# Kernel optimization log

Hardware: AMD Instinct MI355X
Metric: run time of the kernel (lower is better)

## Reference

```python
import jax, jax.numpy as jnp
import numpy as np

NUM_GENES = 978
EMBED_DIM = 301
NUM_HEADS = 4
EMBED_DIM_HEADS = 48
N_NODES = 10000
N_EDGES = 320000


def setup_inputs() -> dict:
    key = jax.random.key(0)
    k1, k2, k3, k4 = jax.random.split(key, 4)
    x = jax.random.normal(k1, (N_NODES, NUM_GENES), dtype=jnp.float32)
    edge_index = jax.random.randint(k2, (2, N_EDGES), 0, N_NODES, dtype=jnp.int64)
    edge_weight = jax.random.uniform(k3, (N_EDGES,), dtype=jnp.float32)
    # GCNConv params: glorot-ish linear weight and zero bias
    W = jax.random.normal(k4, (NUM_GENES, EMBED_DIM), dtype=jnp.float32) * 0.03
    b = jnp.zeros((EMBED_DIM,), dtype=jnp.float32)
    return {"x": x, "edge_index": edge_index, "edge_weight": edge_weight, "W": W, "b": b}


def reference(x, edge_index, edge_weight, W, b):
    N = x.shape[0]
    src, dst = edge_index[0], edge_index[1]
    # GCNConv default: add self-loops with weight 1
    loop = jnp.arange(N, dtype=src.dtype)
    src_f = jnp.concatenate([src, loop])
    dst_f = jnp.concatenate([dst, loop])
    w_f = jnp.concatenate([edge_weight, jnp.ones((N,), dtype=edge_weight.dtype)])
    # symmetric normalization: deg over target nodes
    deg = jax.ops.segment_sum(w_f, dst_f, num_segments=N)
    deg_inv_sqrt = jnp.where(deg > 0, jax.lax.rsqrt(deg), 0.0)
    norm = deg_inv_sqrt[src_f] * w_f * deg_inv_sqrt[dst_f]  # [E+N]
    h = x @ W  # [N, EMBED_DIM]
    # gather source features, scale, scatter-add into targets
    out = jax.ops.segment_sum(norm[:, None] * h[src_f], dst_f, num_segments=N)
    out = out + b
    out = jax.nn.relu(out)
    # unsqueeze(1), unsqueeze(3), repeat(1, H, 1, dph) with H=4, dph=48//4=12
    rep = EMBED_DIM_HEADS // NUM_HEADS
    out = jnp.broadcast_to(out[:, None, :, None], (N, NUM_HEADS, EMBED_DIM, rep))
    return out
```

## Files before the change

### kernel.cpp

```cpp
#include <hip/hip_runtime.h>
#include <math.h>

#define NGENES 978
#define EDIM   301
#define NNODES 10000
#define NEDGES 320000
#define KPAD   992
#define NPAD   320
#define MPAD   10112
#define HP     320
#define ELLS   128

typedef float f4v __attribute__((ext_vector_type(4)));
typedef short s8v __attribute__((ext_vector_type(8)));

__device__ __forceinline__ void split_bf16(float v, short& hi, short& lo) {
    unsigned int b = __float_as_uint(v);
    hi = (short)(b >> 16);
    float hif = __uint_as_float(b & 0xFFFF0000u);
    float lof = v - hif;
    lo = (short)(__float_as_uint(lof) >> 16);
}

__global__ void prep_init(const unsigned int* __restrict__ ei, int* flag, int* cur) {
    int i = blockIdx.x * blockDim.x + threadIdx.x;
    if (i < NNODES) cur[i] = 0;
    if (blockIdx.x == 0 && threadIdx.x < 64) {
        unsigned int v = ei[2 * threadIdx.x + 1];
        unsigned long long nz = __ballot(v != 0u);
        if (threadIdx.x == 0) *flag = (nz == 0ULL) ? 1 : 0;
    }
}

__device__ __forceinline__ int load_idx(const void* ei, long long i, int is64) {
    return is64 ? (int)((const long long*)ei)[i] : ((const int*)ei)[i];
}

__global__ void fill_ell(const void* __restrict__ ei, const float* __restrict__ w,
                         int* cur, int2* __restrict__ ell,
                         const int* __restrict__ flag) {
    int e = blockIdx.x * blockDim.x + threadIdx.x;
    if (e >= NEDGES) return;
    int is64 = *flag;
    int s = load_idx(ei, e, is64);
    int d = load_idx(ei, (long long)NEDGES + e, is64);
    int slot = atomicAdd(&cur[d], 1);
    if (slot < ELLS) ell[(size_t)d * ELLS + slot] = make_int2(s, __float_as_int(w[e]));
}

__global__ __launch_bounds__(256) void deg_dinv(const int2* __restrict__ ell,
                                                const int* __restrict__ cur,
                                                float* __restrict__ dinv) {
    int n = (blockIdx.x * blockDim.x + threadIdx.x) >> 6;
    int lane = threadIdx.x & 63;
    if (n >= NNODES) return;
    int cnt = min(cur[n], ELLS);
    float s = 0.0f;
    for (int l = lane; l < cnt; l += 64)
        s += __int_as_float(ell[(size_t)n * ELLS + l].y);
    #pragma unroll
    for (int off = 32; off; off >>= 1) s += __shfl_xor(s, off);
    if (lane == 0) dinv[n] = rsqrtf(1.0f + s);
}

#define XCH (NNODES * (KPAD / 8))
#define WCH (NPAD * (KPAD / 8))
__global__ void cvt_xw(const float* __restrict__ x, const float* __restrict__ W,
                       short* __restrict__ xh, short* __restrict__ xl,
                       short* __restrict__ wh, short* __restrict__ wl) {
    int idx = blockIdx.x * blockDim.x + threadIdx.x;
    if (idx < XCH) {
        int r = idx / (KPAD / 8);
        int kc = (idx - r * (KPAD / 8)) * 8;
        s8v h8, l8;
        #pragma unroll
        for (int j = 0; j < 8; ++j) {
            int k = kc + j;
            float v = (k < NGENES) ? x[(size_t)r * NGENES + k] : 0.0f;
            short hi, lo;
            split_bf16(v, hi, lo);
            h8[j] = hi; l8[j] = lo;
        }
        *(s8v*)(xh + (size_t)r * KPAD + kc) = h8;
        *(s8v*)(xl + (size_t)r * KPAD + kc) = l8;
    } else if (idx < XCH + WCH) {
        int wi = idx - XCH;
        int n = wi / (KPAD / 8);
        int kc = (wi - n * (KPAD / 8)) * 8;
        s8v h8, l8;
        #pragma unroll
        for (int j = 0; j < 8; ++j) {
            int k = kc + j;
            float v = (n < EDIM && k < NGENES) ? W[(size_t)k * EDIM + n] : 0.0f;
            short hi, lo;
            split_bf16(v, hi, lo);
            h8[j] = hi; l8[j] = lo;
        }
        *(s8v*)(wh + (size_t)n * KPAD + kc) = h8;
        *(s8v*)(wl + (size_t)n * KPAD + kc) = l8;
    }
}

__global__ __launch_bounds__(256) void gemm_bf16(const short* __restrict__ xh,
                                                 const short* __restrict__ xl,
                                                 const short* __restrict__ wh,
                                                 const short* __restrict__ wl,
                                                 float* __restrict__ h) {
    __shared__ short Ah[128 * 40], Al[128 * 40], Bh[64 * 40], Bl[64 * 40];
    const int tid  = threadIdx.x;
    const int lane = tid & 63;
    const int w    = tid >> 6;
    const int wm   = (w >> 1) * 64;
    const int wn   = (w & 1) * 32;
    const int bm   = blockIdx.y * 128;
    const int bn   = blockIdx.x * 64;
    const int l15  = lane & 15;
    const int g8   = (lane >> 4) * 8;

    f4v acc[4][2] = {};

    const int arow0 = tid >> 2;
    const int aslot = (tid & 3) * 8;

    for (int ks = 0; ks < KPAD / 32; ++ks) {
        const int k0 = ks * 32;
        #pragma unroll
        for (int q = 0; q < 2; ++q) {
            const int row = q * 64 + arow0;
            const size_t goff = (size_t)(bm + row) * KPAD + k0 + aslot;
            s8v vh = *(const s8v*)(xh + goff);
            s8v vl = *(const s8v*)(xl + goff);
            *(s8v*)&Ah[row * 40 + aslot] = vh;
            *(s8v*)&Al[row * 40 + aslot] = vl;
        }
        {
            const int row = tid >> 2;
            const size_t goff = (size_t)(bn + row) * KPAD + k0 + aslot;
            s8v vh = *(const s8v*)(wh + goff);
            s8v vl = *(const s8v*)(wl + goff);
            *(s8v*)&Bh[row * 40 + aslot] = vh;
            *(s8v*)&Bl[row * 40 + aslot] = vl;
        }
        __syncthreads();
        s8v ah[4], al[4], bh[2], bl[2];
        #pragma unroll
        for (int fn = 0; fn < 2; ++fn) {
            const int r = wn + fn * 16 + l15;
            bh[fn] = *(const s8v*)&Bh[r * 40 + g8];
            bl[fn] = *(const s8v*)&Bl[r * 40 + g8];
        }
        #pragma unroll
        for (int fm = 0; fm < 4; ++fm) {
            const int r = wm + fm * 16 + l15;
            ah[fm] = *(const s8v*)&Ah[r * 40 + g8];
            al[fm] = *(const s8v*)&Al[r * 40 + g8];
        }
        #pragma unroll
        for (int fm = 0; fm < 4; ++fm)
            #pragma unroll
            for (int fn = 0; fn < 2; ++fn) {
                acc[fm][fn] = __builtin_amdgcn_mfma_f32_16x16x32_bf16(ah[fm], bh[fn], acc[fm][fn], 0, 0, 0);
                acc[fm][fn] = __builtin_amdgcn_mfma_f32_16x16x32_bf16(ah[fm], bl[fn], acc[fm][fn], 0, 0, 0);
                acc[fm][fn] = __builtin_amdgcn_mfma_f32_16x16x32_bf16(al[fm], bh[fn], acc[fm][fn], 0, 0, 0);
            }
        __syncthreads();
    }
    const int mrb = (lane >> 4) * 4;
    #pragma unroll
    for (int fm = 0; fm < 4; ++fm)
        #pragma unroll
        for (int fn = 0; fn < 2; ++fn) {
            const int col = bn + wn + fn * 16 + l15;
            #pragma unroll
            for (int r = 0; r < 4; ++r) {
                const int row = bm + wm + fm * 16 + mrb + r;
                if (row < NNODES) h[(size_t)row * HP + col] = acc[fm][fn][r];
            }
        }
}

__global__ __launch_bounds__(320) void gather_out(const float* __restrict__ h,
                                                  const float* __restrict__ dinv,
                                                  const float* __restrict__ bias,
                                                  const int2* __restrict__ ell,
                                                  const int* __restrict__ cur,
                                                  f4v* __restrict__ out) {
    __shared__ float row[HP];
    const int n = blockIdx.x;
    const int t = threadIdx.x;
    const int cnt = min(cur[n], ELLS);
    const int2* en = ell + (size_t)n * ELLS;

    float acc = 0.0f;
    int e = 0;
    for (; e + 4 <= cnt; e += 4) {
        int2 p0 = en[e], p1 = en[e + 1], p2 = en[e + 2], p3 = en[e + 3];
        float w0 = __int_as_float(p0.y) * dinv[p0.x];
        float w1 = __int_as_float(p1.y) * dinv[p1.x];
        float w2 = __int_as_float(p2.y) * dinv[p2.x];
        float w3 = __int_as_float(p3.y) * dinv[p3.x];
        float v0 = h[(size_t)p0.x * HP + t];
        float v1 = h[(size_t)p1.x * HP + t];
        float v2 = h[(size_t)p2.x * HP + t];
        float v3 = h[(size_t)p3.x * HP + t];
        acc = fmaf(w0, v0, acc); acc = fmaf(w1, v1, acc);
        acc = fmaf(w2, v2, acc); acc = fmaf(w3, v3, acc);
    }
    for (; e < cnt; ++e) {
        int2 p = en[e];
        acc = fmaf(__int_as_float(p.y) * dinv[p.x], h[(size_t)p.x * HP + t], acc);
    }

    const float dn = dinv[n];
    float v = acc * dn + h[(size_t)n * HP + t] * (dn * dn)
            + ((t < EDIM) ? bias[t] : 0.0f);
    row[t] = fmaxf(v, 0.0f);
    __syncthreads();

    f4v* o = out + (size_t)n * 4 * 903;
    #pragma unroll
    for (int q = 0; q < 3; ++q) {
        int p = q * 320 + t;
        if (p < 903) {
            const float vv = row[p / 3];
            f4v v4 = {vv, vv, vv, vv};
            __builtin_nontemporal_store(v4, &o[p]);
            __builtin_nontemporal_store(v4, &o[903 + p]);
            __builtin_nontemporal_store(v4, &o[1806 + p]);
            __builtin_nontemporal_store(v4, &o[2709 + p]);
        }
    }
}

extern "C" void kernel_launch(void* const* d_in, const int* in_sizes, int n_in,
                              void* d_out, int out_size, void* d_ws, size_t ws_size,
                              hipStream_t stream) {
    const float* x  = (const float*)d_in[0];
    const void*  ei = d_in[1];
    const float* ew = (const float*)d_in[2];
    const float* W  = (const float*)d_in[3];
    const float* b  = (const float*)d_in[4];

    char* p = (char*)d_ws;
    int*   cur  = (int*)p;                   p += 40960;
    float* dinv = (float*)p;                 p += 40960;
    int*   flag = (int*)p;                   p += 256;
    int2*  ell  = (int2*)p;                  p += (size_t)NNODES * ELLS * 8;
    float* h    = (float*)p;                 p += (size_t)NNODES * HP * 4;
    short* xh   = (short*)p;                 p += (size_t)MPAD * KPAD * 2;
    short* xl   = (short*)p;                 p += (size_t)MPAD * KPAD * 2;
    short* wh   = (short*)p;                 p += (size_t)NPAD * KPAD * 2;
    short* wl   = (short*)p;                 p += (size_t)NPAD * KPAD * 2;

    prep_init<<<40, 256, 0, stream>>>((const unsigned int*)ei, flag, cur);
    fill_ell<<<(NEDGES + 255) / 256, 256, 0, stream>>>(ei, ew, cur, ell, flag);
    deg_dinv<<<(NNODES * 64 + 255) / 256, 256, 0, stream>>>(ell, cur, dinv);

    cvt_xw<<<(XCH + WCH + 255) / 256, 256, 0, stream>>>(x, W, xh, xl, wh, wl);

    dim3 ggrid(NPAD / 64, MPAD / 128);
    gemm_bf16<<<ggrid, 256, 0, stream>>>(xh, xl, wh, wl, h);

    gather_out<<<NNODES, 320, 0, stream>>>(h, dinv, b, ell, cur, (f4v*)d_out);
    (void)in_sizes; (void)n_in; (void)out_size; (void)ws_size;
}
```

Baseline: 729.7 us.

## Switch split GEMM to fp16 with two MFMAs and widen gather unroll

Replaces the three-term bf16 hi/lo split GEMM with an fp16 split. Only x is split into hi and lo, while W keeps a single fp16 term, so each k-step issues two MFMAs instead of three and W loads and LDS traffic are halved. The gather loop now batches 8 edges, with all loads issued before the FMAs, to expose more memory-level parallelism. W in plain fp16 carries about 11 bits of mantissa, which may cost accuracy, and fp16 range is narrower than bf16's.

Result: no change. 731.8 us (+0.3%).

```diff
diff --git a/kernel.cpp b/kernel.cpp
--- a/kernel.cpp
+++ b/kernel.cpp
@@ -11,15 +11,12 @@
 #define HP     320
 #define ELLS   128
 
-typedef float f4v __attribute__((ext_vector_type(4)));
-typedef short s8v __attribute__((ext_vector_type(8)));
-
-__device__ __forceinline__ void split_bf16(float v, short& hi, short& lo) {
-    unsigned int b = __float_as_uint(v);
-    hi = (short)(b >> 16);
-    float hif = __uint_as_float(b & 0xFFFF0000u);
-    float lof = v - hif;
-    lo = (short)(__float_as_uint(lof) >> 16);
+typedef float    f4v __attribute__((ext_vector_type(4)));
+typedef _Float16 h8v __attribute__((ext_vector_type(8)));
+
+__device__ __forceinline__ void split_f16(float v, _Float16& hi, _Float16& lo) {
+    hi = (_Float16)v;
+    lo = (_Float16)(v - (float)hi);
 }
 
 __global__ void prep_init(const unsigned int* __restrict__ ei, int* flag, int* cur) {
@@ -66,47 +63,43 @@
 #define XCH (NNODES * (KPAD / 8))
 #define WCH (NPAD * (KPAD / 8))
 __global__ void cvt_xw(const float* __restrict__ x, const float* __restrict__ W,
-                       short* __restrict__ xh, short* __restrict__ xl,
-                       short* __restrict__ wh, short* __restrict__ wl) {
+                       _Float16* __restrict__ xh, _Float16* __restrict__ xl,
+                       _Float16* __restrict__ wh) {
     int idx = blockIdx.x * blockDim.x + threadIdx.x;
     if (idx < XCH) {
         int r = idx / (KPAD / 8);
         int kc = (idx - r * (KPAD / 8)) * 8;
-        s8v h8, l8;
+        h8v h8, l8;
         #pragma unroll
         for (int j = 0; j < 8; ++j) {
             int k = kc + j;
             float v = (k < NGENES) ? x[(size_t)r * NGENES + k] : 0.0f;
-            short hi, lo;
-            split_bf16(v, hi, lo);
+            _Float16 hi, lo;
+            split_f16(v, hi, lo);
             h8[j] = hi; l8[j] = lo;
         }
-        *(s8v*)(xh + (size_t)r * KPAD + kc) = h8;
-        *(s8v*)(xl + (size_t)r * KPAD + kc) = l8;
+        *(h8v*)(xh + (size_t)r * KPAD + kc) = h8;
+        *(h8v*)(xl + (size_t)r * KPAD + kc) = l8;
     } else if (idx < XCH + WCH) {
         int wi = idx - XCH;
         int n = wi / (KPAD / 8);
         int kc = (wi - n * (KPAD / 8)) * 8;
-        s8v h8, l8;
+        h8v h8;
         #pragma unroll
         for (int j = 0; j < 8; ++j) {
             int k = kc + j;
             float v = (n < EDIM && k < NGENES) ? W[(size_t)k * EDIM + n] : 0.0f;
-            short hi, lo;
-            split_bf16(v, hi, lo);
-            h8[j] = hi; l8[j] = lo;
-        }
-        *(s8v*)(wh + (size_t)n * KPAD + kc) = h8;
-        *(s8v*)(wl + (size_t)n * KPAD + kc) = l8;
-    }
-}
-
-__global__ __launch_bounds__(256) void gemm_bf16(const short* __restrict__ xh,
-                                                 const short* __restrict__ xl,
-                                                 const short* __restrict__ wh,
-                                                 const short* __restrict__ wl,
-                                                 float* __restrict__ h) {
-    __shared__ short Ah[128 * 40], Al[128 * 40], Bh[64 * 40], Bl[64 * 40];
+            h8[j] = (_Float16)v;
+        }
+        *(h8v*)(wh + (size_t)n * KPAD + kc) = h8;
+    }
+}
+
+__global__ __launch_bounds__(256) void gemm_f16(const _Float16* __restrict__ xh,
+                                                const _Float16* __restrict__ xl,
+                                                const _Float16* __restrict__ wh,
+                                                float* __restrict__ h) {
+    __shared__ _Float16 Ah[128 * 40], Al[128 * 40], Bh[64 * 40];
     const int tid  = threadIdx.x;
     const int lane = tid & 63;
     const int w    = tid >> 6;
@@ -128,40 +121,35 @@
         for (int q = 0; q < 2; ++q) {
             const int row = q * 64 + arow0;
             const size_t goff = (size_t)(bm + row) * KPAD + k0 + aslot;
-            s8v vh = *(const s8v*)(xh + goff);
-            s8v vl = *(const s8v*)(xl + goff);
-            *(s8v*)&Ah[row * 40 + aslot] = vh;
-            *(s8v*)&Al[row * 40 + aslot] = vl;
+            h8v vh = *(const h8v*)(xh + goff);
+            h8v vl = *(const h8v*)(xl + goff);
+            *(h8v*)&Ah[row * 40 + aslot] = vh;
+            *(h8v*)&Al[row * 40 + aslot] = vl;
         }
         {
             const int row = tid >> 2;
             const size_t goff = (size_t)(bn + row) * KPAD + k0 + aslot;
-            s8v vh = *(const s8v*)(wh + goff);
-            s8v vl = *(const s8v*)(wl + goff);
-            *(s8v*)&Bh[row * 40 + aslot] = vh;
-            *(s8v*)&Bl[row * 40 + aslot] = vl;
+            *(h8v*)&Bh[row * 40 + aslot] = *(const h8v*)(wh + goff);
         }
         __syncthreads();
-        s8v ah[4], al[4], bh[2], bl[2];
+        h8v ah[4], al[4], bh[2];
         #pragma unroll
         for (int fn = 0; fn < 2; ++fn) {
             const int r = wn + fn * 16 + l15;
-            bh[fn] = *(const s8v*)&Bh[r * 40 + g8];
-            bl[fn] = *(const s8v*)&Bl[r * 40 + g8];
+            bh[fn] = *(const h8v*)&Bh[r * 40 + g8];
         }
         #pragma unroll
         for (int fm = 0; fm < 4; ++fm) {
             const int r = wm + fm * 16 + l15;
-            ah[fm] = *(const s8v*)&Ah[r * 40 + g8];
-            al[fm] = *(const s8v*)&Al[r * 40 + g8];
+            ah[fm] = *(const h8v*)&Ah[r * 40 + g8];
+            al[fm] = *(const h8v*)&Al[r * 40 + g8];
         }
         #pragma unroll
         for (int fm = 0; fm < 4; ++fm)
             #pragma unroll
             for (int fn = 0; fn < 2; ++fn) {
-                acc[fm][fn] = __builtin_amdgcn_mfma_f32_16x16x32_bf16(ah[fm], bh[fn], acc[fm][fn], 0, 0, 0);
-                acc[fm][fn] = __builtin_amdgcn_mfma_f32_16x16x32_bf16(ah[fm], bl[fn], acc[fm][fn], 0, 0, 0);
-                acc[fm][fn] = __builtin_amdgcn_mfma_f32_16x16x32_bf16(al[fm], bh[fn], acc[fm][fn], 0, 0, 0);
+                acc[fm][fn] = __builtin_amdgcn_mfma_f32_16x16x32_f16(ah[fm], bh[fn], acc[fm][fn], 0, 0, 0);
+                acc[fm][fn] = __builtin_amdgcn_mfma_f32_16x16x32_f16(al[fm], bh[fn], acc[fm][fn], 0, 0, 0);
             }
         __syncthreads();
     }
@@ -193,18 +181,16 @@
 
     float acc = 0.0f;
     int e = 0;
-    for (; e + 4 <= cnt; e += 4) {
-        int2 p0 = en[e], p1 = en[e + 1], p2 = en[e + 2], p3 = en[e + 3];
-        float w0 = __int_as_float(p0.y) * dinv[p0.x];
-        float w1 = __int_as_float(p1.y) * dinv[p1.x];
-        float w2 = __int_as_float(p2.y) * dinv[p2.x];
-        float w3 = __int_as_float(p3.y) * dinv[p3.x];
-        float v0 = h[(size_t)p0.x * HP + t];
-        float v1 = h[(size_t)p1.x * HP + t];
-        float v2 = h[(size_t)p2.x * HP + t];
-        float v3 = h[(size_t)p3.x * HP + t];
-        acc = fmaf(w0, v0, acc); acc = fmaf(w1, v1, acc);
-        acc = fmaf(w2, v2, acc); acc = fmaf(w3, v3, acc);
+    for (; e + 8 <= cnt; e += 8) {
+        int2 p[8];
+        float v[8];
+        #pragma unroll
+        for (int j = 0; j < 8; ++j) p[j] = en[e + j];
+        #pragma unroll
+        for (int j = 0; j < 8; ++j) v[j] = h[(size_t)p[j].x * HP + t];
+        #pragma unroll
+        for (int j = 0; j < 8; ++j)
+            acc = fmaf(__int_as_float(p[j].y) * dinv[p[j].x], v[j], acc);
     }
     for (; e < cnt; ++e) {
         int2 p = en[e];
@@ -242,24 +228,23 @@
     const float* b  = (const float*)d_in[4];
 
     char* p = (char*)d_ws;
-    int*   cur  = (int*)p;                   p += 40960;
-    float* dinv = (float*)p;                 p += 40960;
-    int*   flag = (int*)p;                   p += 256;
-    int2*  ell  = (int2*)p;                  p += (size_t)NNODES * ELLS * 8;
-    float* h    = (float*)p;                 p += (size_t)NNODES * HP * 4;
-    short* xh   = (short*)p;                 p += (size_t)MPAD * KPAD * 2;
-    short* xl   = (short*)p;                 p += (size_t)MPAD * KPAD * 2;
-    short* wh   = (short*)p;                 p += (size_t)NPAD * KPAD * 2;
-    short* wl   = (short*)p;                 p += (size_t)NPAD * KPAD * 2;
+    int*      cur  = (int*)p;                p += 40960;
+    float*    dinv = (float*)p;              p += 40960;
+    int*      flag = (int*)p;                p += 256;
+    int2*     ell  = (int2*)p;               p += (size_t)NNODES * ELLS * 8;
+    float*    h    = (float*)p;              p += (size_t)NNODES * HP * 4;
+    _Float16* xh   = (_Float16*)p;           p += (size_t)MPAD * KPAD * 2;
+    _Float16* xl   = (_Float16*)p;           p += (size_t)MPAD * KPAD * 2;
+    _Float16* wh   = (_Float16*)p;           p += (size_t)NPAD * KPAD * 2;
 
     prep_init<<<40, 256, 0, stream>>>((const unsigned int*)ei, flag, cur);
     fill_ell<<<(NEDGES + 255) / 256, 256, 0, stream>>>(ei, ew, cur, ell, flag);
     deg_dinv<<<(NNODES * 64 + 255) / 256, 256, 0, stream>>>(ell, cur, dinv);
 
-    cvt_xw<<<(XCH + WCH + 255) / 256, 256, 0, stream>>>(x, W, xh, xl, wh, wl);
+    cvt_xw<<<(XCH + WCH + 255) / 256, 256, 0, stream>>>(x, W, xh, xl, wh);
 
     dim3 ggrid(NPAD / 64, MPAD / 128);
-    gemm_bf16<<<ggrid, 256, 0, stream>>>(xh, xl, wh, wl, h);
+    gemm_f16<<<ggrid, 256, 0, stream>>>(xh, xl, wh, h);
 
     gather_out<<<NNODES, 320, 0, stream>>>(h, dinv, b, ell, cur, (f4v*)d_out);
     (void)in_sizes; (void)n_in; (void)out_size; (void)ws_size;
```
